# Kernel tuning notes

Hardware: AMD Instinct MI355X
Metric: run time of the kernel (lower is better)

The kernel has to match this reference:

```python
import jax, jax.numpy as jnp
import numpy as np

B, N, C, H = 8, 1024, 768, 12
HD = C // H
SCALE = HD ** -0.5
# iRPE 'product' config with ratio=1.9 (official get_rpe_config defaults)
ALPHA, BETA, GAMMA = 1.9, 3.8, 15.2
BETA_INT = int(BETA)          # 3
S = 2 * BETA_INT + 1          # 7 buckets per axis
NB = S * S                    # 49 buckets total


def _piecewise_index(d):
    # iRPE piecewise index: identity near zero, log-spaced further out, clipped at beta.
    d = d.astype(np.float64)
    ad = np.abs(d)
    far = np.sign(d) * np.clip(
        np.round(ALPHA + np.log(np.maximum(ad, 1e-6) / ALPHA) / np.log(GAMMA / ALPHA) * (BETA - ALPHA)),
        a_min=None, a_max=BETA)
    return np.where(ad <= ALPHA, np.round(d), far).astype(np.int64)


def _rp_bucket(n):
    # 2D 'product' relative-position buckets on a sqrt(n) x sqrt(n) grid.
    side = int(np.sqrt(n))
    ys, xs = np.divmod(np.arange(n), side)
    r = _piecewise_index(ys[:, None] - ys[None, :]) + BETA_INT  # [0, 2*beta_int]
    c = _piecewise_index(xs[:, None] - xs[None, :]) + BETA_INT
    return (r * S + c).astype(np.int32)  # [N, N] in [0, NB)


def setup_inputs() -> dict:
    key = jax.random.key(0)
    ks = jax.random.split(key, 8)
    q = jax.random.normal(ks[0], (B, N, C), jnp.float32)
    k = jax.random.normal(ks[1], (B, N, C), jnp.float32)
    v = jax.random.normal(ks[2], (B, N, C), jnp.float32)
    # shared-head contextual RPE tables
    w_rpe_q = jax.random.normal(ks[3], (HD, NB), jnp.float32) * 0.02
    w_rpe_k = jax.random.normal(ks[4], (HD, NB), jnp.float32) * 0.02
    w_rpe_v = jax.random.normal(ks[5], (NB, HD), jnp.float32) * 0.02
    proj_w = jax.random.normal(ks[6], (C, C), jnp.float32) * (C ** -0.5)
    proj_b = jax.random.normal(ks[7], (C,), jnp.float32) * 0.01
    rp_bucket = jnp.asarray(_rp_bucket(N))
    return dict(q=q, k=k, v=v, w_rpe_q=w_rpe_q, w_rpe_k=w_rpe_k,
                w_rpe_v=w_rpe_v, proj_w=proj_w, proj_b=proj_b, rp_bucket=rp_bucket)


def _gather_rows(t, rp_bucket):
    # t: [B,H,N,NB] -> bias[B,H,N,N]; bias[..., i, j] = t[..., i, rp_bucket[i, j]]
    rows = jnp.arange(t.shape[2])[:, None]
    return t[:, :, rows, rp_bucket]


def reference(q, k, v, w_rpe_q, w_rpe_k, w_rpe_v, proj_w, proj_b, rp_bucket):
    qh = q.reshape(B, N, H, HD).transpose(0, 2, 1, 3)  # [B,H,N,HD]
    kh = k.reshape(B, N, H, HD).transpose(0, 2, 1, 3)
    vh = v.reshape(B, N, H, HD).transpose(0, 2, 1, 3)
    attn = jnp.einsum('bhid,bhjd->bhij', qh, kh) * SCALE
    # rpe_k: q_i . W_k[:, bucket(i,j)]
    attn = attn + _gather_rows(jnp.einsum('bhid,du->bhiu', qh, w_rpe_k), rp_bucket)
    # rpe_q: (scale*k_j) . W_q[:, bucket(j,i)], then transposed onto (i,j)
    attn = attn + _gather_rows(jnp.einsum('bhjd,du->bhju', kh * SCALE, w_rpe_q), rp_bucket).swapaxes(2, 3)
    attn = jax.nn.softmax(attn, axis=-1)
    out = jnp.einsum('bhij,bhjd->bhid', attn, vh)
    # rpe_v: out_i += sum_j attn[i,j] * W_v[bucket(i,j)] via per-row bucket segment sums
    rows = jnp.arange(N)[:, None]
    bucket_sums = jnp.zeros((B, H, N, NB), attn.dtype).at[:, :, rows, rp_bucket].add(attn)
    out = out + jnp.einsum('bhiu,ud->bhid', bucket_sums, w_rpe_v)
    out = out.transpose(0, 2, 1, 3).reshape(B, N, C)
    out = out @ proj_w.T + proj_b
    return out, attn
```

## Files before the change

kernel.cpp:

```cpp
#include <hip/hip_runtime.h>

#define B_ 8
#define N_ 1024
#define C_ 768
#define H_ 12
#define HD_ 64
#define NB_ 49
#define BH_ 96
#define SCALE_ 0.125f

typedef unsigned int u32;
typedef unsigned short u16;
typedef __attribute__((ext_vector_type(8))) short mfrag;
typedef __attribute__((ext_vector_type(4))) float f32x4;
typedef __attribute__((ext_vector_type(4))) u32 u32x4;

__device__ __forceinline__ u16 f2bf(float x) {
    u32 u = __float_as_uint(x);
    u32 r = u + 0x7FFFu + ((u >> 16) & 1u);
    return (u16)(r >> 16);
}
__device__ __forceinline__ float bf2f(u16 h) { return __uint_as_float(((u32)h) << 16); }

__device__ __forceinline__ int lutf(int d) {
    int a = d < 0 ? -d : d;
    int gg = (a < 2 ? a : 2) + (a >= 4 ? 1 : 0);
    return d < 0 ? 3 - gg : 3 + gg;
}

__global__ void irpe_prep_k(const float* __restrict__ q, const float* __restrict__ k,
                            const float* __restrict__ w_rpe_q, const float* __restrict__ w_rpe_k,
                            u16* __restrict__ qh, u16* __restrict__ ql,
                            u16* __restrict__ kh, u16* __restrict__ kl,
                            float* __restrict__ tk, u16* __restrict__ tqT) {
    const int bh = blockIdx.y, b = bh / H_, h = bh % H_;
    const int row0 = blockIdx.x * 4;
    __shared__ float qs[4][HD_], ks[4][HD_];
    const int t = threadIdx.x;
    {
        const int r = t >> 6, d = t & 63;
        const size_t gi = ((size_t)(b * N_ + row0 + r)) * C_ + h * HD_ + d;
        const float vq = q[gi], vk = k[gi];
        qs[r][d] = vq;
        ks[r][d] = vk;
        const size_t so = (((size_t)(bh << 10)) + row0 + r) * 64 + d;
        const u16 qhi = f2bf(vq), khi = f2bf(vk);
        qh[so] = qhi; ql[so] = f2bf(vq - bf2f(qhi));
        kh[so] = khi; kl[so] = f2bf(vk - bf2f(khi));
    }
    __syncthreads();
    if (t < 4 * NB_) {
        const int r = t / NB_, u = t - r * NB_;
        float dk = 0.f, dq = 0.f;
#pragma unroll
        for (int d = 0; d < HD_; ++d) {
            dk = fmaf(qs[r][d], w_rpe_k[d * NB_ + u], dk);
            dq = fmaf(ks[r][d], w_rpe_q[d * NB_ + u], dq);
        }
        tk[((size_t)bh * N_ + row0 + r) * NB_ + u] = dk;
        tqT[(((size_t)bh * NB_ + u) << 10) + row0 + r] = f2bf(dq * SCALE_);
    }
}

__global__ void irpe_prep_w_k(const float* __restrict__ W,
                              u16* __restrict__ wh, u16* __restrict__ wl) {
    const int o = (blockIdx.x * 256 + threadIdx.x) * 4;
    const float4 x = *(const float4*)&W[o];
    const u16 h0 = f2bf(x.x), h1 = f2bf(x.y), h2 = f2bf(x.z), h3 = f2bf(x.w);
    *(ushort4*)&wh[o] = make_ushort4(h0, h1, h2, h3);
    *(ushort4*)&wl[o] = make_ushort4(f2bf(x.x - bf2f(h0)), f2bf(x.y - bf2f(h1)),
                                     f2bf(x.z - bf2f(h2)), f2bf(x.w - bf2f(h3)));
}

__global__ void irpe_vt_k(const float* __restrict__ v, u16* __restrict__ vth) {
    __shared__ float tile[64][65];
    const int bh = blockIdx.y, jc0 = blockIdx.x * 64;
    const int b = bh / H_, h = bh % H_;
    const int t = threadIdx.x;
#pragma unroll
    for (int rep = 0; rep < 4; ++rep) {
        const int fl = rep * 256 + t;
        const int jr = fl >> 4, c4 = (fl & 15) * 4;
        const float4 x = *(const float4*)&v[((size_t)(b * N_ + jc0 + jr)) * C_ + h * HD_ + c4];
        tile[jr][c4] = x.x; tile[jr][c4 + 1] = x.y; tile[jr][c4 + 2] = x.z; tile[jr][c4 + 3] = x.w;
    }
    __syncthreads();
    const int d = t >> 2, jq = (t & 3) * 16;
    u32 ph[8];
#pragma unroll
    for (int jj = 0; jj < 8; ++jj) {
        const u16 h0 = f2bf(tile[jq + jj * 2][d]);
        const u16 h1 = f2bf(tile[jq + jj * 2 + 1][d]);
        ph[jj] = (u32)h0 | ((u32)h1 << 16);
    }
    const size_t dst = (((size_t)bh * 64 + d) << 10) + jc0 + jq;
    *(uint4*)&vth[dst] = make_uint4(ph[0], ph[1], ph[2], ph[3]);
    *(uint4*)&vth[dst + 8] = make_uint4(ph[4], ph[5], ph[6], ph[7]);
}

__global__ __launch_bounds__(256, 3) void irpe_attn_mfma_k(
    const u16* __restrict__ qh_g, const u16* __restrict__ ql_g,
    const u16* __restrict__ kh_g, const u16* __restrict__ kl_g,
    const u16* __restrict__ vth_g,
    const float* __restrict__ tk, const u16* __restrict__ tqT,
    u16* __restrict__ e_g, float* __restrict__ s_arr, float* __restrict__ pre) {
    __shared__ u16 kAh[4096], kAl[4096];
    __shared__ u16 vAh[4096];
    __shared__ u16 awh[4096];
    __shared__ u16 tq_su[NB_ * 72];
    __shared__ u16 tks_s[64 * 50];

    const int gid = blockIdx.x;
    const int xcd = gid & 7, L = gid >> 3;
    const int bh = xcd * 12 + (L >> 4);
    const int itile = L & 15;
    const int b = bh / H_, h = bh % H_;
    const int i0 = itile * 64;
    const int t = threadIdx.x;
    const int w = t >> 6, lane = t & 63;
    const int ln4 = lane >> 4, lh15 = lane & 15;
    const int yi = itile * 2 + (w >> 1);
    const size_t tqbase = (size_t)bh * NB_ * 1024;
    const int arow0 = (bh << 10) + i0;

    mfrag qAh[2], qAl[2];
#pragma unroll
    for (int ks = 0; ks < 2; ++ks) {
        const size_t qa = (((size_t)(bh << 10) + i0 + w * 16 + lh15) << 6) + (ln4 << 3) + (ks << 5);
        qAh[ks] = *(const mfrag*)&qh_g[qa];
        qAl[ks] = *(const mfrag*)&ql_g[qa];
    }

    int bxp[2][4];
#pragma unroll
    for (int jh = 0; jh < 2; ++jh)
#pragma unroll
        for (int r = 0; r < 4; ++r) {
            const int xi = (w & 1) * 16 + ln4 * 4 + r;
            bxp[jh][r] = lutf(xi - (jh * 16 + lh15));
        }

    mfrag kstg[4], vstg[2];
#pragma unroll
    for (int rep = 0; rep < 2; ++rep) {
        const int unit = rep * 256 + t;
        const int row = unit >> 3, un = unit & 7;
        const size_t ka = (((size_t)(bh << 10) + row) << 6) + un * 8;
        kstg[rep * 2] = *(const mfrag*)&kh_g[ka];
        kstg[rep * 2 + 1] = *(const mfrag*)&kl_g[ka];
        vstg[rep] = *(const mfrag*)&vth_g[(((size_t)(bh * 64) + row) << 10) + un * 8];
    }
    u32x4 tqpre[2];
    {
        const int u0 = t >> 3, c0 = t & 7;
        tqpre[0] = *(const u32x4*)&tqT[tqbase + ((size_t)u0 << 10) + c0 * 8];
        if (t < 136) {
            const int u1 = (256 + t) >> 3, c1 = t & 7;
            tqpre[1] = *(const u32x4*)&tqT[tqbase + ((size_t)u1 << 10) + c1 * 8];
        }
    }

    {
        const size_t tkb = ((size_t)(bh << 10) + i0) * NB_;
        for (int idx = t; idx < 64 * NB_; idx += 256) {
            const int row = idx / NB_, u = idx - row * NB_;
            tks_s[row * 50 + u] = f2bf(tk[tkb + idx]);
        }
    }

    f32x4 apv[4] = {{0.f, 0.f, 0.f, 0.f}, {0.f, 0.f, 0.f, 0.f},
                    {0.f, 0.f, 0.f, 0.f}, {0.f, 0.f, 0.f, 0.f}};
    float srow[4] = {0.f, 0.f, 0.f, 0.f};

#pragma unroll 1
    for (int ch = 0; ch < 16; ++ch) {
        const int jc0 = ch << 6;

#pragma unroll
        for (int rep = 0; rep < 2; ++rep) {
            const int unit = rep * 256 + t;
            const int row = unit >> 3, un = unit & 7;
            const int ldso = row * 128 + ((un ^ (row & 7)) << 4);
            *(mfrag*)((char*)kAh + ldso) = kstg[rep * 2];
            *(mfrag*)((char*)kAl + ldso) = kstg[rep * 2 + 1];
            *(mfrag*)((char*)vAh + ldso) = vstg[rep];
        }
        {
            const int u0 = t >> 3, c0 = t & 7;
            *(u32x4*)((char*)tq_su + u0 * 144 + c0 * 16) = tqpre[0];
            if (t < 136) {
                const int u1 = (256 + t) >> 3;
                *(u32x4*)((char*)tq_su + u1 * 144 + (t & 7) * 16) = tqpre[1];
            }
        }
        __syncthreads();

        f32x4 aq[4];
        __builtin_amdgcn_s_setprio(1);
#pragma unroll
        for (int ji = 0; ji < 4; ++ji) {
            const int rb = ji * 16 + lh15, swb = rb & 7;
            const mfrag bh0 = *(const mfrag*)((const char*)kAh + rb * 128 + ((ln4 ^ swb) << 4));
            const mfrag bl0 = *(const mfrag*)((const char*)kAl + rb * 128 + ((ln4 ^ swb) << 4));
            const mfrag bh1 = *(const mfrag*)((const char*)kAh + rb * 128 + (((4 + ln4) ^ swb) << 4));
            const mfrag bl1 = *(const mfrag*)((const char*)kAl + rb * 128 + (((4 + ln4) ^ swb) << 4));
            f32x4 c = {0.f, 0.f, 0.f, 0.f};
            c = __builtin_amdgcn_mfma_f32_16x16x32_bf16(qAh[0], bh0, c, 0, 0, 0);
            c = __builtin_amdgcn_mfma_f32_16x16x32_bf16(qAh[0], bl0, c, 0, 0, 0);
            c = __builtin_amdgcn_mfma_f32_16x16x32_bf16(qAl[0], bh0, c, 0, 0, 0);
            c = __builtin_amdgcn_mfma_f32_16x16x32_bf16(qAh[1], bh1, c, 0, 0, 0);
            c = __builtin_amdgcn_mfma_f32_16x16x32_bf16(qAh[1], bl1, c, 0, 0, 0);
            c = __builtin_amdgcn_mfma_f32_16x16x32_bf16(qAl[1], bh1, c, 0, 0, 0);
            aq[ji] = c;
        }
        __builtin_amdgcn_s_setprio(0);

        if (ch < 15) {
            const int jc1 = jc0 + 64;
#pragma unroll
            for (int rep = 0; rep < 2; ++rep) {
                const int unit = rep * 256 + t;
                const int row = unit >> 3, un = unit & 7;
                const size_t ka = (((size_t)(bh << 10) + jc1 + row) << 6) + un * 8;
                kstg[rep * 2] = *(const mfrag*)&kh_g[ka];
                kstg[rep * 2 + 1] = *(const mfrag*)&kl_g[ka];
                vstg[rep] = *(const mfrag*)&vth_g[(((size_t)(bh * 64) + row) << 10) + jc1 + un * 8];
            }
            const int u0 = t >> 3, c0 = t & 7;
            tqpre[0] = *(const u32x4*)&tqT[tqbase + ((size_t)u0 << 10) + jc1 + c0 * 8];
            if (t < 136) {
                const int u1 = (256 + t) >> 3;
                tqpre[1] = *(const u32x4*)&tqT[tqbase + ((size_t)u1 << 10) + jc1 + (t & 7) * 8];
            }
        }

#pragma unroll
        for (int ji = 0; ji < 4; ++ji) {
            const int yj = (ch << 1) + (ji >> 1);
            const int by7 = 7 * lutf(yi - yj);
            const int jl = ji * 16 + lh15;
#pragma unroll
            for (int r = 0; r < 4; ++r) {
                const int il = w * 16 + ln4 * 4 + r;
                const int bij = by7 + bxp[ji & 1][r];
                const float e = __expf(fmaf(aq[ji][r], SCALE_,
                                            bf2f(tks_s[il * 50 + bij]) + bf2f(tq_su[(48 - bij) * 72 + jl])));
                srow[r] += e;
                const int off = il * 128 + ((jl << 1) ^ ((il & 7) << 4));
                *(u16*)((char*)awh + off) = f2bf(e);
            }
        }

        {
            const int rowA = w * 16 + lh15, sa = (rowA & 7) << 4;
            mfrag pah[2];
#pragma unroll
            for (int ks = 0; ks < 2; ++ks)
                pah[ks] = *(const mfrag*)((const char*)awh + rowA * 128 + ((((ln4 << 4) + (ks << 6))) ^ sa));
            __builtin_amdgcn_s_setprio(1);
#pragma unroll
            for (int di = 0; di < 4; ++di) {
                const int rv = di * 16 + lh15, swv = rv & 7;
                const mfrag vh0 = *(const mfrag*)((const char*)vAh + rv * 128 + ((ln4 ^ swv) << 4));
                const mfrag vh1 = *(const mfrag*)((const char*)vAh + rv * 128 + (((4 + ln4) ^ swv) << 4));
                f32x4 c = apv[di];
                c = __builtin_amdgcn_mfma_f32_16x16x32_bf16(pah[0], vh0, c, 0, 0, 0);
                c = __builtin_amdgcn_mfma_f32_16x16x32_bf16(pah[1], vh1, c, 0, 0, 0);
                apv[di] = c;
            }
            __builtin_amdgcn_s_setprio(0);
        }

#pragma unroll
        for (int rep = 0; rep < 2; ++rep) {
            const int unit = rep * 64 + lane;
            const int rowl = unit >> 3, un = unit & 7;
            const int row = w * 16 + rowl;
            const u32x4 val = *(const u32x4*)((const char*)awh + row * 128 + ((un << 4) ^ ((row & 7) << 4)));
            __builtin_nontemporal_store(val,
                (u32x4*)&e_g[((size_t)(arow0 + row) << 11) + jc0 + un * 8]);
        }
        __syncthreads();
    }

    float inv[4];
#pragma unroll
    for (int r = 0; r < 4; ++r) {
        float s = srow[r];
        s += __shfl_xor(s, 1); s += __shfl_xor(s, 2);
        s += __shfl_xor(s, 4); s += __shfl_xor(s, 8);
        inv[r] = 1.0f / s;
        if (lh15 == 0) s_arr[((size_t)bh << 10) + i0 + w * 16 + ln4 * 4 + r] = s;
    }

#pragma unroll
    for (int di = 0; di < 4; ++di) {
        const int d = di * 16 + lh15;
#pragma unroll
        for (int r = 0; r < 4; ++r) {
            const int i = i0 + w * 16 + ln4 * 4 + r;
            pre[((size_t)(b * N_ + i)) * C_ + h * HD_ + d] = apv[di][r] * inv[r];
        }
    }
}

__global__ __launch_bounds__(256) void irpe_rescale_fuse_k(
    float* __restrict__ attn, const float* __restrict__ s_arr,
    const float* __restrict__ pre, const float* __restrict__ w_rpe_v,
    u16* __restrict__ preh, u16* __restrict__ prel) {
    __shared__ float R[8][32][8];
    __shared__ float wv[NB_ * 64];
    __shared__ float bss[8][52];
    __shared__ float inv_s[8];
    __shared__ int lutyj[32];

    const int gid = blockIdx.x;
    const int xcd = gid & 7, loc = gid >> 3;
    const int bh = xcd * 12 + (loc >> 7);
    const int i0 = (loc & 127) * 8;
    const int b = bh / H_, h = bh % H_;
    const int t = threadIdx.x;
    const int w = t >> 6, lane = t & 63;
    const int yi2 = i0 >> 5;

    for (int idx = t; idx < 8 * 32 * 8; idx += 256) ((float*)R)[idx] = 0.f;
    for (int idx = t; idx < NB_ * 64; idx += 256) wv[idx] = w_rpe_v[idx];
    if (t < 8) inv_s[t] = 1.0f / s_arr[((size_t)bh << 10) + i0 + t];
    if (t < 32) lutyj[t] = lutf(yi2 - t);
    __syncthreads();

    const int j0 = lane * 16;
    const int yj = j0 >> 5;
    const int xb = j0 & 31;

#pragma unroll
    for (int rp = 0; rp < 2; ++rp) {
        const int rr = rp * 4 + w;
        const int i = i0 + rr;
        const int xi = i & 31;
        const float inv = inv_s[rr];
        const u16* erow = (const u16*)attn + (((size_t)((bh << 10) + i)) << 11);
        const u32x4 ea = *(const u32x4*)&erow[j0];
        const u32x4 eb = *(const u32x4*)&erow[j0 + 8];
        float ev[16];
        {
            const u32 wds[8] = {ea.x, ea.y, ea.z, ea.w, eb.x, eb.y, eb.z, eb.w};
#pragma unroll
            for (int m = 0; m < 8; ++m) {
                ev[2 * m] = bf2f((u16)(wds[m] & 0xFFFFu));
                ev[2 * m + 1] = bf2f((u16)(wds[m] >> 16));
            }
        }

        float acc = 0.f;
        int cur = lutf(xi - xb);
#pragma unroll
        for (int c = 0; c < 16; ++c) {
            const int bx_ = lutf(xi - (xb + c));
            if (bx_ != cur) { atomicAdd(&R[rr][yj][cur], acc); acc = 0.f; cur = bx_; }
            acc += ev[c];
        }
        atomicAdd(&R[rr][yj][cur], acc);

        float* rowf = &attn[((size_t)((bh << 10) + i)) << 10];
#pragma unroll
        for (int m = 0; m < 4; ++m) {
            const f32x4 o = {ev[4 * m] * inv, ev[4 * m + 1] * inv,
                             ev[4 * m + 2] * inv, ev[4 * m + 3] * inv};
            *(f32x4*)&rowf[j0 + 4 * m] = o;
        }
    }
    __syncthreads();

    for (int idx = t; idx < 8 * NB_; idx += 256) {
        const int rr = idx / NB_, u = idx - rr * NB_;
        const int by = u / 7, bx = u - by * 7;
        float s = 0.f;
#pragma unroll
        for (int yj2 = 0; yj2 < 32; ++yj2)
            if (lutyj[yj2] == by) s += R[rr][yj2][bx];
        bss[rr][u] = s * inv_s[rr];
    }
    __syncthreads();

    for (int idx = t; idx < 512; idx += 256) {
        const int rr = idx >> 6, d = idx & 63;
        const size_t row = (size_t)(b * N_ + i0 + rr);
        float acc = pre[row * C_ + h * HD_ + d];
        for (int u = 0; u < NB_; ++u) acc = fmaf(bss[rr][u], wv[u * 64 + d], acc);
        const u16 hi = f2bf(acc);
        preh[row * C_ + h * HD_ + d] = hi;
        prel[row * C_ + h * HD_ + d] = f2bf(acc - bf2f(hi));
    }
}

__global__ __launch_bounds__(256, 4) void irpe_proj_mfma_k(
    const u16* __restrict__ Ah_g, const u16* __restrict__ Al_g,
    const u16* __restrict__ Bh_g, const u16* __restrict__ Bl_g,
    const float* __restrict__ bias, float* __restrict__ Cout) {
    __shared__ u16 Ah[4096], Al[4096], Bh[4096], Bl[4096];
    const int bm = blockIdx.x * 64, bn = blockIdx.y * 64;
    const int t = threadIdx.x;
    const int w = t >> 6, lane = t & 63;
    const int ln4 = lane >> 4, lh15 = lane & 15;

    f32x4 acc[4] = {{0.f, 0.f, 0.f, 0.f}, {0.f, 0.f, 0.f, 0.f},
                    {0.f, 0.f, 0.f, 0.f}, {0.f, 0.f, 0.f, 0.f}};
    float bias_r[4];
#pragma unroll
    for (int ji = 0; ji < 4; ++ji) bias_r[ji] = bias[bn + ji * 16 + lh15];

    const int srow_ = t >> 3, sun = t & 7;
    const int ldso = srow_ * 128 + ((sun ^ (srow_ & 7)) << 4);

    for (int kt = 0; kt < C_; kt += 64) {
#pragma unroll
        for (int rep = 0; rep < 2; ++rep) {
            const int row = rep * 32 + srow_;
            const int ldo = ldso + rep * 32 * 128;
            const size_t ao = (size_t)(bm + row) * C_ + kt + sun * 8;
            const size_t bo = (size_t)(bn + row) * C_ + kt + sun * 8;
            *(u32x4*)((char*)Ah + ldo) = *(const u32x4*)&Ah_g[ao];
            *(u32x4*)((char*)Al + ldo) = *(const u32x4*)&Al_g[ao];
            *(u32x4*)((char*)Bh + ldo) = *(const u32x4*)&Bh_g[bo];
            *(u32x4*)((char*)Bl + ldo) = *(const u32x4*)&Bl_g[bo];
        }
        __syncthreads();

        const int ra = w * 16 + lh15, sa = ra & 7;
        const mfrag aF0h = *(const mfrag*)((const char*)Ah + ra * 128 + ((ln4 ^ sa) << 4));
        const mfrag aF0l = *(const mfrag*)((const char*)Al + ra * 128 + ((ln4 ^ sa) << 4));
        const mfrag aF1h = *(const mfrag*)((const char*)Ah + ra * 128 + (((4 + ln4) ^ sa) << 4));
        const mfrag aF1l = *(const mfrag*)((const char*)Al + ra * 128 + (((4 + ln4) ^ sa) << 4));
        __builtin_amdgcn_s_setprio(1);
#pragma unroll
        for (int ji = 0; ji < 4; ++ji) {
            const int rb = ji * 16 + lh15, sb = rb & 7;
            const mfrag bF0h = *(const mfrag*)((const char*)Bh + rb * 128 + ((ln4 ^ sb) << 4));
            const mfrag bF0l = *(const mfrag*)((const char*)Bl + rb * 128 + ((ln4 ^ sb) << 4));
            const mfrag bF1h = *(const mfrag*)((const char*)Bh + rb * 128 + (((4 + ln4) ^ sb) << 4));
            const mfrag bF1l = *(const mfrag*)((const char*)Bl + rb * 128 + (((4 + ln4) ^ sb) << 4));
            f32x4 c = acc[ji];
            c = __builtin_amdgcn_mfma_f32_16x16x32_bf16(aF0h, bF0h, c, 0, 0, 0);
            c = __builtin_amdgcn_mfma_f32_16x16x32_bf16(aF0h, bF0l, c, 0, 0, 0);
            c = __builtin_amdgcn_mfma_f32_16x16x32_bf16(aF0l, bF0h, c, 0, 0, 0);
            c = __builtin_amdgcn_mfma_f32_16x16x32_bf16(aF1h, bF1h, c, 0, 0, 0);
            c = __builtin_amdgcn_mfma_f32_16x16x32_bf16(aF1h, bF1l, c, 0, 0, 0);
            c = __builtin_amdgcn_mfma_f32_16x16x32_bf16(aF1l, bF1h, c, 0, 0, 0);
            acc[ji] = c;
        }
        __builtin_amdgcn_s_setprio(0);
        __syncthreads();
    }

#pragma unroll
    for (int ji = 0; ji < 4; ++ji) {
        const int col = bn + ji * 16 + lh15;
#pragma unroll
        for (int r = 0; r < 4; ++r) {
            const int row = bm + w * 16 + ln4 * 4 + r;
            Cout[(size_t)row * C_ + col] = acc[ji][r] + bias_r[ji];
        }
    }
}

extern "C" void kernel_launch(void* const* d_in, const int* in_sizes, int n_in,
                              void* d_out, int out_size, void* d_ws, size_t ws_size,
                              hipStream_t stream) {
    const float* q       = (const float*)d_in[0];
    const float* k       = (const float*)d_in[1];
    const float* v       = (const float*)d_in[2];
    const float* w_rpe_q = (const float*)d_in[3];
    const float* w_rpe_k = (const float*)d_in[4];
    const float* w_rpe_v = (const float*)d_in[5];
    const float* proj_w  = (const float*)d_in[6];
    const float* proj_b  = (const float*)d_in[7];

    float* out  = (float*)d_out;
    float* attn = out + (size_t)B_ * N_ * C_;

    char* ws = (char*)d_ws;
    float* tk    = (float*)ws; ws += (size_t)BH_ * N_ * NB_ * 4;
    u16*   tqT   = (u16*)ws;   ws += (size_t)BH_ * NB_ * N_ * 2;
    float* pre   = (float*)ws; ws += (size_t)B_ * N_ * C_ * 4;
    float* s_arr = (float*)ws; ws += (size_t)BH_ * N_ * 4;
    u16* qh   = (u16*)ws; ws += (size_t)BH_ * N_ * 64 * 2;
    u16* ql   = (u16*)ws; ws += (size_t)BH_ * N_ * 64 * 2;
    u16* kh   = (u16*)ws; ws += (size_t)BH_ * N_ * 64 * 2;
    u16* kl   = (u16*)ws; ws += (size_t)BH_ * N_ * 64 * 2;
    u16* vth  = (u16*)ws; ws += (size_t)BH_ * 64 * N_ * 2;
    u16* preh = (u16*)ws; ws += (size_t)B_ * N_ * C_ * 2;
    u16* prel = (u16*)ws; ws += (size_t)B_ * N_ * C_ * 2;
    u16* wh   = (u16*)ws; ws += (size_t)C_ * C_ * 2;
    u16* wl   = (u16*)ws; ws += (size_t)C_ * C_ * 2;

    irpe_prep_k<<<dim3(N_ / 4, BH_), 256, 0, stream>>>(q, k, w_rpe_q, w_rpe_k,
                                                       qh, ql, kh, kl, tk, tqT);
    irpe_prep_w_k<<<(C_ * C_) / 1024, 256, 0, stream>>>(proj_w, wh, wl);
    irpe_vt_k<<<dim3(16, BH_), 256, 0, stream>>>(v, vth);

    irpe_attn_mfma_k<<<BH_ * (N_ / 64), 256, 0, stream>>>(
        qh, ql, kh, kl, vth, tk, tqT, (u16*)attn, s_arr, pre);

    irpe_rescale_fuse_k<<<BH_ * (N_ / 8), 256, 0, stream>>>(attn, s_arr, pre,
                                                            w_rpe_v, preh, prel);
    irpe_proj_mfma_k<<<dim3((B_ * N_) / 64, C_ / 64), 256, 0, stream>>>(
        preh, prel, wh, wl, proj_b, out);
}
```

Before: 565.5 us.

## Double attention row tile to 128 with 512-thread blocks to share K/V staging

The attention kernel now processes 128 query rows per block with 8 waves (512 threads) instead of 64 rows with 4 waves. Each K/V/tq chunk is loaded and staged once into shared memory and used by twice as many waves, halving global K/V traffic per query row. Each thread now issues a single staging load per tensor instead of two. The cost is larger LDS per block (awh and tks_s doubled), a grid half the size (768 blocks), and more threads waiting at each barrier, which may reduce occupancy or latency hiding.

```diff
diff --git a/kernel.cpp b/kernel.cpp
--- a/kernel.cpp
+++ b/kernel.cpp
@@ -98,7 +98,7 @@
     *(uint4*)&vth[dst + 8] = make_uint4(ph[4], ph[5], ph[6], ph[7]);
 }
 
-__global__ __launch_bounds__(256, 3) void irpe_attn_mfma_k(
+__global__ __launch_bounds__(512, 4) void irpe_attn_mfma_k(
     const u16* __restrict__ qh_g, const u16* __restrict__ ql_g,
     const u16* __restrict__ kh_g, const u16* __restrict__ kl_g,
     const u16* __restrict__ vth_g,
@@ -106,20 +106,20 @@
     u16* __restrict__ e_g, float* __restrict__ s_arr, float* __restrict__ pre) {
     __shared__ u16 kAh[4096], kAl[4096];
     __shared__ u16 vAh[4096];
-    __shared__ u16 awh[4096];
+    __shared__ u16 awh[8192];
     __shared__ u16 tq_su[NB_ * 72];
-    __shared__ u16 tks_s[64 * 50];
+    __shared__ u16 tks_s[128 * 50];
 
     const int gid = blockIdx.x;
     const int xcd = gid & 7, L = gid >> 3;
-    const int bh = xcd * 12 + (L >> 4);
-    const int itile = L & 15;
+    const int bh = xcd * 12 + (L >> 3);
+    const int itile = L & 7;
     const int b = bh / H_, h = bh % H_;
-    const int i0 = itile * 64;
+    const int i0 = itile * 128;
     const int t = threadIdx.x;
     const int w = t >> 6, lane = t & 63;
     const int ln4 = lane >> 4, lh15 = lane & 15;
-    const int yi = itile * 2 + (w >> 1);
+    const int yi = itile * 4 + (w >> 1);
     const size_t tqbase = (size_t)bh * NB_ * 1024;
     const int arow0 = (bh << 10) + i0;
 
@@ -140,29 +140,21 @@
             bxp[jh][r] = lutf(xi - (jh * 16 + lh15));
         }
 
-    mfrag kstg[4], vstg[2];
-#pragma unroll
-    for (int rep = 0; rep < 2; ++rep) {
-        const int unit = rep * 256 + t;
-        const int row = unit >> 3, un = unit & 7;
-        const size_t ka = (((size_t)(bh << 10) + row) << 6) + un * 8;
-        kstg[rep * 2] = *(const mfrag*)&kh_g[ka];
-        kstg[rep * 2 + 1] = *(const mfrag*)&kl_g[ka];
-        vstg[rep] = *(const mfrag*)&vth_g[(((size_t)(bh * 64) + row) << 10) + un * 8];
-    }
-    u32x4 tqpre[2];
+    const int srow = t >> 3, sun = t & 7;
+    const int ldso = srow * 128 + ((sun ^ (srow & 7)) << 4);
+    mfrag kstg0, kstg1, vstg;
     {
-        const int u0 = t >> 3, c0 = t & 7;
-        tqpre[0] = *(const u32x4*)&tqT[tqbase + ((size_t)u0 << 10) + c0 * 8];
-        if (t < 136) {
-            const int u1 = (256 + t) >> 3, c1 = t & 7;
-            tqpre[1] = *(const u32x4*)&tqT[tqbase + ((size_t)u1 << 10) + c1 * 8];
-        }
-    }
+        const size_t ka = (((size_t)(bh << 10) + srow) << 6) + sun * 8;
+        kstg0 = *(const mfrag*)&kh_g[ka];
+        kstg1 = *(const mfrag*)&kl_g[ka];
+        vstg = *(const mfrag*)&vth_g[(((size_t)(bh * 64) + srow) << 10) + sun * 8];
+    }
+    u32x4 tqpre;
+    if (t < 392) tqpre = *(const u32x4*)&tqT[tqbase + ((size_t)srow << 10) + sun * 8];
 
     {
         const size_t tkb = ((size_t)(bh << 10) + i0) * NB_;
-        for (int idx = t; idx < 64 * NB_; idx += 256) {
+        for (int idx = t; idx < 128 * NB_; idx += 512) {
             const int row = idx / NB_, u = idx - row * NB_;
             tks_s[row * 50 + u] = f2bf(tk[tkb + idx]);
         }
@@ -170,29 +162,16 @@
 
     f32x4 apv[4] = {{0.f, 0.f, 0.f, 0.f}, {0.f, 0.f, 0.f, 0.f},
                     {0.f, 0.f, 0.f, 0.f}, {0.f, 0.f, 0.f, 0.f}};
-    float srow[4] = {0.f, 0.f, 0.f, 0.f};
+    float srow_sum[4] = {0.f, 0.f, 0.f, 0.f};
 
 #pragma unroll 1
     for (int ch = 0; ch < 16; ++ch) {
         const int jc0 = ch << 6;
 
-#pragma unroll
-        for (int rep = 0; rep < 2; ++rep) {
-            const int unit = rep * 256 + t;
-            const int row = unit >> 3, un = unit & 7;
-            const int ldso = row * 128 + ((un ^ (row & 7)) << 4);
-            *(mfrag*)((char*)kAh + ldso) = kstg[rep * 2];
-            *(mfrag*)((char*)kAl + ldso) = kstg[rep * 2 + 1];
-            *(mfrag*)((char*)vAh + ldso) = vstg[rep];
-        }
-        {
-            const int u0 = t >> 3, c0 = t & 7;
-            *(u32x4*)((char*)tq_su + u0 * 144 + c0 * 16) = tqpre[0];
-            if (t < 136) {
-                const int u1 = (256 + t) >> 3;
-                *(u32x4*)((char*)tq_su + u1 * 144 + (t & 7) * 16) = tqpre[1];
-            }
-        }
+        *(mfrag*)((char*)kAh + ldso) = kstg0;
+        *(mfrag*)((char*)kAl + ldso) = kstg1;
+        *(mfrag*)((char*)vAh + ldso) = vstg;
+        if (t < 392) *(u32x4*)((char*)tq_su + srow * 144 + sun * 16) = tqpre;
         __syncthreads();
 
         f32x4 aq[4];
@@ -217,21 +196,11 @@
 
         if (ch < 15) {
             const int jc1 = jc0 + 64;
-#pragma unroll
-            for (int rep = 0; rep < 2; ++rep) {
-                const int unit = rep * 256 + t;
-                const int row = unit >> 3, un = unit & 7;
-                const size_t ka = (((size_t)(bh << 10) + jc1 + row) << 6) + un * 8;
-                kstg[rep * 2] = *(const mfrag*)&kh_g[ka];
-                kstg[rep * 2 + 1] = *(const mfrag*)&kl_g[ka];
-                vstg[rep] = *(const mfrag*)&vth_g[(((size_t)(bh * 64) + row) << 10) + jc1 + un * 8];
-            }
-            const int u0 = t >> 3, c0 = t & 7;
-            tqpre[0] = *(const u32x4*)&tqT[tqbase + ((size_t)u0 << 10) + jc1 + c0 * 8];
-            if (t < 136) {
-                const int u1 = (256 + t) >> 3;
-                tqpre[1] = *(const u32x4*)&tqT[tqbase + ((size_t)u1 << 10) + jc1 + (t & 7) * 8];
-            }
+            const size_t ka = (((size_t)(bh << 10) + jc1 + srow) << 6) + sun * 8;
+            kstg0 = *(const mfrag*)&kh_g[ka];
+            kstg1 = *(const mfrag*)&kl_g[ka];
+            vstg = *(const mfrag*)&vth_g[(((size_t)(bh * 64) + srow) << 10) + jc1 + sun * 8];
+            if (t < 392) tqpre = *(const u32x4*)&tqT[tqbase + ((size_t)srow << 10) + jc1 + sun * 8];
         }
 
 #pragma unroll
@@ -245,7 +214,7 @@
                 const int bij = by7 + bxp[ji & 1][r];
                 const float e = __expf(fmaf(aq[ji][r], SCALE_,
                                             bf2f(tks_s[il * 50 + bij]) + bf2f(tq_su[(48 - bij) * 72 + jl])));
-                srow[r] += e;
+                srow_sum[r] += e;
                 const int off = il * 128 + ((jl << 1) ^ ((il & 7) << 4));
                 *(u16*)((char*)awh + off) = f2bf(e);
             }
@@ -286,7 +255,7 @@
     float inv[4];
 #pragma unroll
     for (int r = 0; r < 4; ++r) {
-        float s = srow[r];
+        float s = srow_sum[r];
         s += __shfl_xor(s, 1); s += __shfl_xor(s, 2);
         s += __shfl_xor(s, 4); s += __shfl_xor(s, 8);
         inv[r] = 1.0f / s;
@@ -499,7 +468,7 @@
     irpe_prep_w_k<<<(C_ * C_) / 1024, 256, 0, stream>>>(proj_w, wh, wl);
     irpe_vt_k<<<dim3(16, BH_), 256, 0, stream>>>(v, vth);
 
-    irpe_attn_mfma_k<<<BH_ * (N_ / 64), 256, 0, stream>>>(
+    irpe_attn_mfma_k<<<BH_ * 8, 512, 0, stream>>>(
         qh, ql, kh, kl, vth, tk, tqT, (u16*)attn, s_arr, pre);
 
     irpe_rescale_fuse_k<<<BH_ * (N_ / 8), 256, 0, stream>>>(attn, s_arr, pre,
```

Measured after the change: 593.6 us. +5.0%, slower.
